# Kernel tuning notes

Hardware: AMD Instinct MI355X
Metric: run time of the kernel (lower is better)

Reference implementation:

```python
import jax, jax.numpy as jnp
import numpy as np

BN_EPS = 1e-5

def _conv(x, w, b, pad):
    # x [B,C,H,W], w [O,I,kh,kw]
    y = jax.lax.conv_general_dilated(x, w, window_strides=(1, 1),
                                     padding=[(pad, pad), (pad, pad)],
                                     dimension_numbers=('NCHW', 'OIHW', 'NCHW'))
    return y + b[None, :, None, None]

def _bn(x, p):
    # p [4,C] rows: gamma, beta, running_mean, running_var (inference-mode BN)
    g, b, m, v = p
    scale = (g * jax.lax.rsqrt(v + BN_EPS))[None, :, None, None]
    return (x - m[None, :, None, None]) * scale + b[None, :, None, None]

def _up2_bilinear_ac(x):
    # UpsamplingBilinear2d(scale_factor=2) == bilinear, align_corners=True
    def interp(x, axis):
        n = x.shape[axis]
        out = 2 * n
        c = jnp.arange(out, dtype=x.dtype) * ((n - 1) / (out - 1))
        i0 = jnp.floor(c).astype(jnp.int32)
        i1 = jnp.minimum(i0 + 1, n - 1)
        w = c - i0.astype(x.dtype)
        sh = [1] * x.ndim
        sh[axis] = out
        w = w.reshape(sh)
        return jnp.take(x, i0, axis=axis) * (1 - w) + jnp.take(x, i1, axis=axis) * w
    return interp(interp(x, 2), 3)

def _dilate(x, k, iterations):
    # cv2.dilate with ones(k,k) kernel == sliding-window max (the custom-kernel target);
    # get_open_map detaches, hence stop_gradient.
    for _ in range(iterations):
        x = jax.lax.reduce_window(x, -jnp.inf, jax.lax.max,
                                  (1, 1, k, k), (1, 1, 1, 1), 'SAME')
    return jax.lax.stop_gradient(x)

def _pixel_shuffle2(x):
    B, C4, H, W = x.shape
    C = C4 // 4
    x = x.reshape(B, C, 2, 2, H, W).transpose(0, 1, 4, 2, 5, 3)
    return x.reshape(B, C, 2 * H, 2 * W)

def setup_inputs() -> dict:
    key = jax.random.key(0)
    ks = jax.random.split(key, 16)
    B, C1, C2, H, W = 8, 64, 128, 64, 64

    def bn_params(k, C):
        k1, k2, k3, k4 = jax.random.split(k, 4)
        g = jax.random.uniform(k1, (C,)) * 0.5 + 0.75
        b = jax.random.normal(k2, (C,)) * 0.1
        m = jax.random.normal(k3, (C,)) * 0.1
        v = jax.random.uniform(k4, (C,)) + 0.5
        return jnp.stack([g, b, m, v])

    def conv_w(k, o, i, kk):
        return jax.random.normal(k, (o, i, kk, kk)) * 0.05

    return {
        'cur_x': jax.random.normal(ks[0], (B, C1, 2 * H, 2 * W)),
        'dep_x': jax.random.normal(ks[1], (B, C2, H, W)),
        'in_map': jax.random.normal(ks[2], (B, 1, H, W)),
        'up_w': conv_w(ks[3], 4 * C1, C2, 7), 'up_b': jnp.zeros((4 * C1,)),
        'up_bn': bn_params(ks[4], 4 * C1),
        'conv2_w': conv_w(ks[5], C1, C1, 3), 'conv2_b': jnp.zeros((C1,)),
        'd1_w': conv_w(ks[6], C1, C1, 3), 'd1_b': jnp.zeros((C1,)),
        'd1_bn': bn_params(ks[7], C1),
        'd2_w': conv_w(ks[8], C1, C1, 3), 'd2_b': jnp.zeros((C1,)),
        'd2_bn': bn_params(ks[9], C1),
        'd3_w': conv_w(ks[10], C1, C1, 3), 'd3_b': jnp.zeros((C1,)),
        'd3_bn': bn_params(ks[11], C1),
        'out_w': conv_w(ks[12], 1, C1, 7), 'out_b': jnp.zeros((1,)),
        'beta': jnp.ones((1,)),
    }

def reference(cur_x, dep_x, in_map, up_w, up_b, up_bn, conv2_w, conv2_b,
              d1_w, d1_b, d1_bn, d2_w, d2_b, d2_bn, d3_w, d3_b, d3_bn,
              out_w, out_b, beta):
    K, IT = 3, 1  # opr_kernel_size, iterations
    # up + pixel shuffle: [B,C2,H,W] -> [B,C1,2H,2W]
    dep = _pixel_shuffle2(jax.nn.relu(_bn(_conv(dep_x, up_w, up_b, 3), up_bn)))
    in_map1 = 1.0 - in_map
    input_map = jax.nn.sigmoid(_up2_bilinear_ac(in_map))
    input_map1 = jax.nn.sigmoid(_up2_bilinear_ac(in_map1))
    increase_map = _dilate(input_map, K, IT) - input_map
    increase_map1 = _dilate(increase_map, K, IT) - increase_map
    increase_map2 = _dilate(input_map1, K, IT) - input_map1
    outmap = increase_map + increase_map1 + increase_map2
    fn = _conv(outmap * cur_x, conv2_w, conv2_b, 1)
    r = jax.nn.relu(_bn(_conv(dep + beta * fn, d1_w, d1_b, 1), d1_bn))
    r = jax.nn.relu(_bn(_conv(r, d2_w, d2_b, 1), d2_bn))
    r = jax.nn.relu(_bn(_conv(r, d3_w, d3_b, 1), d3_bn))
    output_map = _conv(r, out_w, out_b, 3)
    return (r, output_map)
```

## Files before the change

### kernel.cpp

```cpp
#include <hip/hip_runtime.h>
#include <hip/hip_bf16.h>
#include <math.h>

static __device__ __forceinline__ float sigm(float x) { return 1.0f / (1.0f + expf(-x)); }

static __device__ __forceinline__ short f2bf_s(float f) {
    unsigned u = __float_as_uint(f);
    u += 0x7fffu + ((u >> 16) & 1u);
    return (short)(u >> 16);
}
static __device__ __forceinline__ float bfb2f(short s) {
    return __uint_as_float(((unsigned)(unsigned short)s) << 16);
}

typedef __attribute__((ext_vector_type(8))) short short8;
typedef __attribute__((ext_vector_type(4))) short short4v;
typedef __attribute__((ext_vector_type(4))) float f32x4;

__global__ __launch_bounds__(256) void k_maps(const float* __restrict__ in_map,
                                              short* __restrict__ om_bf) {
    __shared__ float s_u[20][20];
    __shared__ float s_inc[18][18];
    int tid = threadIdx.x;
    int b = blockIdx.z;
    int ty0 = (blockIdx.x >> 3) << 4, tx0 = (blockIdx.x & 7) << 4;
    const float* p = in_map + (b << 12);
    const float s = 63.0f / 127.0f;
    for (int e = tid; e < 400; e += 256) {
        int yy = e / 20, xx = e % 20;
        int gy = ty0 + yy - 2, gx = tx0 + xx - 2;
        float v = 0.0f;
        if ((unsigned)gy < 128u && (unsigned)gx < 128u) {
            float cy = gy * s, cx = gx * s;
            int iy0 = (int)cy, ix0 = (int)cx;
            float wy = cy - (float)iy0, wx = cx - (float)ix0;
            int iy1 = min(iy0 + 1, 63), ix1 = min(ix0 + 1, 63);
            float v00 = p[(iy0 << 6) + ix0], v01 = p[(iy0 << 6) + ix1];
            float v10 = p[(iy1 << 6) + ix0], v11 = p[(iy1 << 6) + ix1];
            v = (1.0f - wy) * ((1.0f - wx) * v00 + wx * v01) +
                wy          * ((1.0f - wx) * v10 + wx * v11);
        }
        s_u[yy][xx] = v;
    }
    __syncthreads();
    for (int e = tid; e < 324; e += 256) {
        int yy = e / 18, xx = e % 18;
        int gy = ty0 + yy - 1, gx = tx0 + xx - 1;
        float val = -INFINITY;
        if ((unsigned)gy < 128u && (unsigned)gx < 128u) {
            float uc = s_u[yy + 1][xx + 1];
            float mx = -INFINITY;
            for (int dy = -1; dy <= 1; ++dy) {
                int ny = gy + dy; if ((unsigned)ny >= 128u) continue;
                for (int dx = -1; dx <= 1; ++dx) {
                    int nx = gx + dx; if ((unsigned)nx >= 128u) continue;
                    mx = fmaxf(mx, s_u[yy + 1 + dy][xx + 1 + dx]);
                }
            }
            val = sigm(mx) - sigm(uc);
        }
        s_inc[yy][xx] = val;
    }
    __syncthreads();
    int row = tid >> 4, col = tid & 15;
    int gy = ty0 + row, gx = tx0 + col;
    float mx = -INFINITY;
    #pragma unroll
    for (int dy = 0; dy < 3; ++dy)
        #pragma unroll
        for (int dx = 0; dx < 3; ++dx)
            mx = fmaxf(mx, s_inc[row + dy][col + dx]);
    float uc = s_u[row + 2][col + 2];
    float mn = INFINITY;
    for (int dy = -1; dy <= 1; ++dy) {
        int ny = gy + dy; if ((unsigned)ny >= 128u) continue;
        for (int dx = -1; dx <= 1; ++dx) {
            int nx = gx + dx; if ((unsigned)nx >= 128u) continue;
            mn = fminf(mn, s_u[row + 2 + dy][col + 2 + dx]);
        }
    }
    float inc2 = sigm(1.0f - mn) - sigm(1.0f - uc);
    om_bf[(b << 14) + (gy << 7) + gx] = f2bf_s(mx + inc2);
}

__global__ __launch_bounds__(256) void k_premult(const float* __restrict__ cur_x,
                                                 const short* __restrict__ om_bf,
                                                 short* __restrict__ xin2) {
    int e = blockIdx.x * 256 + threadIdx.x;
    int flat = e << 2;
    int pix = flat & 16383;
    int b = flat >> 20;
    f32x4 xv = *(const f32x4*)&cur_x[flat];
    short4v ov = *(const short4v*)&om_bf[(b << 14) + pix];
    short4v res;
    #pragma unroll
    for (int k = 0; k < 4; ++k) res[k] = f2bf_s(xv[k] * bfb2f(ov[k]));
    *(short4v*)&xin2[flat] = res;
}

__global__ __launch_bounds__(256) void k_prepw3(const float* __restrict__ w0,
                                                const float* __restrict__ w1,
                                                const float* __restrict__ w2,
                                                const float* __restrict__ w3,
                                                short* __restrict__ wb3) {
    int s = blockIdx.x * 256 + threadIdx.x;
    if (s >= 147456) return;
    int layer = s / 36864; int r = s - layer * 36864;
    const float* w = (layer == 0) ? w0 : (layer == 1) ? w1 : (layer == 2) ? w2 : w3;
    int o = r / 576; int rem = r - o * 576;
    int c = rem / 9; int t = rem - c * 9;
    int dy = t / 3, dx = t - dy * 3;
    int cc = c >> 5, cl = c & 31;
    wb3[layer * 36864 + (((cc * 3 + dy) * 3 + dx) * 64 + o) * 32 + cl] = f2bf_s(w[r]);
}

__global__ __launch_bounds__(256) void k_prepw(const float* __restrict__ w,
                                               short* __restrict__ wb) {
    int s = blockIdx.x * 256 + threadIdx.x;
    if (s >= 1605632) return;
    int O = s / 6272; int r = s - O * 6272;
    int C = r / 49;   int T = r - C * 49;
    int dy = T / 7, dx = T - dy * 7;
    int nt = O >> 6, o = O & 63;
    int cc = C >> 5, c = C & 31;
    int W = ((((nt * 4 + cc) * 7 + dy) * 7 + dx) * 64 + o) * 32 + c;
    wb[W] = f2bf_s(w[s]);
}

__global__ __launch_bounds__(512) void k_upconv_mfma(
    const float* __restrict__ x,
    const short* __restrict__ wb,
    const float* __restrict__ cb,
    const float* __restrict__ bnp,
    short* __restrict__ dep) {
    __shared__ __attribute__((aligned(16))) short s_in[484 * 40];
    int tid = threadIdx.x;
    int wave = tid >> 6, lane = tid & 63;
    int q = lane >> 4, m = lane & 15;
    int mw = wave & 3, ng = wave >> 2;
    int ty0 = (blockIdx.x >> 2) * 16;
    int tx0 = (blockIdx.x & 3) * 16;
    int nt = blockIdx.y;
    int b = blockIdx.z;
    f32x4 acc[4][2];
    #pragma unroll
    for (int i = 0; i < 4; ++i)
        #pragma unroll
        for (int j = 0; j < 2; ++j)
            acc[i][j] = (f32x4){0.f, 0.f, 0.f, 0.f};
    const float* xb = x + ((long)(b * 128) << 12);
    for (int cc = 0; cc < 4; ++cc) {
        __syncthreads();
        for (int e = tid; e < 528; e += 512) {
            int cq = e / 132; int rem = e - cq * 132;
            int yy = rem / 6; int g = rem - yy * 6;
            int gy = ty0 + yy - 3;
            int gx0 = tx0 - 4 + (g << 2);
            bool ok = ((unsigned)gy < 64u) && ((unsigned)gx0 < 64u);
            #pragma unroll
            for (int h = 0; h < 2; ++h) {
                f32x4 v[4];
                if (ok) {
                    const float* src = xb + ((cc * 32 + cq * 8 + h * 4) << 12) + (gy << 6) + gx0;
                    #pragma unroll
                    for (int j2 = 0; j2 < 4; ++j2) v[j2] = *(const f32x4*)(src + (j2 << 12));
                } else {
                    #pragma unroll
                    for (int j2 = 0; j2 < 4; ++j2) v[j2] = (f32x4){0.f, 0.f, 0.f, 0.f};
                }
                #pragma unroll
                for (int t = 0; t < 4; ++t) {
                    int xx = (g << 2) - 1 + t;
                    if ((unsigned)xx < 22u) {
                        short4v pk;
                        #pragma unroll
                        for (int j2 = 0; j2 < 4; ++j2) pk[j2] = f2bf_s(v[j2][t]);
                        *(short4v*)&s_in[(yy * 22 + xx) * 40 + cq * 8 + h * 4] = pk;
                    }
                }
            }
        }
        __syncthreads();
        for (int dy = 0; dy < 7; ++dy) {
            const short* wsl = wb + (((nt * 4 + cc) * 7 + dy) * 7) * 2048;
            #pragma unroll
            for (int dx = 0; dx < 7; ++dx) {
                short8 bf[2];
                #pragma unroll
                for (int j = 0; j < 2; ++j)
                    bf[j] = *(const short8*)(wsl + (dx << 11) + ((ng * 32 + j * 16 + m) << 5) + (q << 3));
                short8 a[4];
                #pragma unroll
                for (int i = 0; i < 4; ++i)
                    a[i] = *(const short8*)&s_in[((mw * 4 + i + dy) * 22 + m + dx) * 40 + q * 8];
                #pragma unroll
                for (int i = 0; i < 4; ++i)
                    #pragma unroll
                    for (int j = 0; j < 2; ++j)
                        acc[i][j] = __builtin_amdgcn_mfma_f32_16x16x32_bf16(
                            a[i], bf[j], acc[i][j], 0, 0, 0);
            }
        }
    }
    #pragma unroll
    for (int j = 0; j < 2; ++j) {
        int o = nt * 64 + ng * 32 + j * 16 + m;
        float g  = bnp[o],       bt = bnp[256 + o];
        float mn = bnp[512 + o], vv = bnp[768 + o];
        float scale = g * rsqrtf(vv + 1e-5f);
        float cbf = cb[o];
        int c = o >> 2, sbit = (o >> 1) & 1, tbit = o & 1;
        #pragma unroll
        for (int i = 0; i < 4; ++i) {
            int y = ty0 + mw * 4 + i;
            #pragma unroll
            for (int reg = 0; reg < 4; ++reg) {
                int xc = tx0 + q * 4 + reg;
                float val = (acc[i][j][reg] + cbf - mn) * scale + bt;
                val = fmaxf(val, 0.0f);
                dep[((b * 64 + c) << 14) + ((2 * y + sbit) << 7) + (2 * xc + tbit)] = f2bf_s(val);
            }
        }
    }
}

template <int MODE, bool OUTBF>
__global__ __launch_bounds__(256) void k_conv3m(
    const short* __restrict__ xin,
    const short* __restrict__ wl,
    const short* __restrict__ dep,
    const float* __restrict__ cb,
    const float* __restrict__ bnp,
    const float* __restrict__ beta,
    void* __restrict__ out) {
    __shared__ __attribute__((aligned(16))) short s_in[180 * 40];
    int tid = threadIdx.x;
    int wave = tid >> 6, lane = tid & 63;
    int q = lane >> 4, m = lane & 15;
    int mw = wave >> 1, nw = wave & 1;
    int ty0 = (blockIdx.x >> 3) * 8;
    int tx0 = (blockIdx.x & 7) * 16;
    int b = blockIdx.z;
    f32x4 acc[4][2];
    #pragma unroll
    for (int i = 0; i < 4; ++i)
        #pragma unroll
        for (int j = 0; j < 2; ++j)
            acc[i][j] = (f32x4){0.f, 0.f, 0.f, 0.f};
    const short* xb = xin + ((long)(b * 64) << 14);
    for (int cc = 0; cc < 2; ++cc) {
        __syncthreads();
        for (int e = tid; e < 240; e += 256) {
            int cq = e / 60; int rem = e - cq * 60;
            int yy = rem / 6; int g = rem - yy * 6;
            int gy = ty0 + yy - 1;
            int gx0 = tx0 - 4 + (g << 2);
            short4v v[8];
            if ((unsigned)gy < 128u && (unsigned)gx0 < 128u) {
                const short* src = xb + ((cc * 32 + cq * 8) << 14) + (gy << 7) + gx0;
                #pragma unroll
                for (int j2 = 0; j2 < 8; ++j2) v[j2] = *(const short4v*)(src + (j2 << 14));
            } else {
                #pragma unroll
                for (int j2 = 0; j2 < 8; ++j2) v[j2] = (short4v){0, 0, 0, 0};
            }
            #pragma unroll
            for (int t = 0; t < 4; ++t) {
                int xx = (g << 2) - 3 + t;
                if ((unsigned)xx < 18u) {
                    short8 pk;
                    #pragma unroll
                    for (int j2 = 0; j2 < 8; ++j2) pk[j2] = v[j2][t];
                    *(short8*)&s_in[(yy * 18 + xx) * 40 + cq * 8] = pk;
                }
            }
        }
        __syncthreads();
        #pragma unroll
        for (int dy = 0; dy < 3; ++dy) {
            #pragma unroll
            for (int dx = 0; dx < 3; ++dx) {
                const short* wp = wl + (((cc * 3 + dy) * 3 + dx) << 11);
                short8 bf[2];
                #pragma unroll
                for (int j = 0; j < 2; ++j)
                    bf[j] = *(const short8*)(wp + ((nw * 32 + j * 16 + m) << 5) + (q << 3));
                short8 a[4];
                #pragma unroll
                for (int i = 0; i < 4; ++i)
                    a[i] = *(const short8*)&s_in[((mw * 4 + i + dy) * 18 + m + dx) * 40 + q * 8];
                #pragma unroll
                for (int i = 0; i < 4; ++i)
                    #pragma unroll
                    for (int j = 0; j < 2; ++j)
                        acc[i][j] = __builtin_amdgcn_mfma_f32_16x16x32_bf16(
                            a[i], bf[j], acc[i][j], 0, 0, 0);
            }
        }
    }
    float betav = (MODE == 1) ? beta[0] : 0.0f;
    #pragma unroll
    for (int j = 0; j < 2; ++j) {
        int o = nw * 32 + j * 16 + m;
        float cbf = cb[o];
        float scale = 1.0f, shift = 0.0f;
        if (MODE == 0) {
            float g  = bnp[o],       bt = bnp[64 + o];
            float mm = bnp[128 + o], vv = bnp[192 + o];
            scale = g * rsqrtf(vv + 1e-5f);
            shift = bt - mm * scale;
        }
        #pragma unroll
        for (int i = 0; i < 4; ++i) {
            int y = ty0 + mw * 4 + i;
            int base = ((b * 64 + o) << 14) + (y << 7) + tx0 + q * 4;
            float vals[4];
            if (MODE == 1) {
                short4v dv = *(const short4v*)&dep[base];
                #pragma unroll
                for (int reg = 0; reg < 4; ++reg)
                    vals[reg] = bfb2f(dv[reg]) + betav * (acc[i][j][reg] + cbf);
            } else {
                #pragma unroll
                for (int reg = 0; reg < 4; ++reg)
                    vals[reg] = fmaxf((acc[i][j][reg] + cbf) * scale + shift, 0.0f);
            }
            if (OUTBF) {
                short4v sv;
                #pragma unroll
                for (int reg = 0; reg < 4; ++reg) sv[reg] = f2bf_s(vals[reg]);
                *(short4v*)((short*)out + base) = sv;
            } else {
                f32x4 fv;
                #pragma unroll
                for (int reg = 0; reg < 4; ++reg) fv[reg] = vals[reg];
                *(f32x4*)((float*)out + base) = fv;
            }
        }
    }
}

__global__ __launch_bounds__(256) void k_outconv(
    const float* __restrict__ r,
    const float* __restrict__ w,
    const float* __restrict__ ob,
    float* __restrict__ out) {
    __shared__ float s_in[8][22][22];
    int tid = threadIdx.x;
    int ty = tid >> 4, tx = tid & 15;
    int ty0 = (blockIdx.x >> 3) << 4, tx0 = (blockIdx.x & 7) << 4;
    int b = blockIdx.z;
    float acc4[4] = {0.f, 0.f, 0.f, 0.f};
    for (int c0 = 0; c0 < 64; c0 += 8) {
        __syncthreads();
        for (int e = tid; e < 8 * 484; e += 256) {
            int i = e / 484; int r2 = e - i * 484; int yy = r2 / 22; int xx = r2 - yy * 22;
            int gy = ty0 + yy - 3, gx = tx0 + xx - 3;
            float v = 0.0f;
            if ((unsigned)gy < 128u && (unsigned)gx < 128u)
                v = r[((b * 64 + c0 + i) << 14) + (gy << 7) + gx];
            s_in[i][yy][xx] = v;
        }
        __syncthreads();
        for (int i = 0; i < 8; ++i) {
            const float* wrow = w + (c0 + i) * 49;
            #pragma unroll
            for (int dy = 0; dy < 7; ++dy)
                #pragma unroll
                for (int dx = 0; dx < 7; ++dx)
                    acc4[i & 3] = fmaf(s_in[i][ty + dy][tx + dx], wrow[dy * 7 + dx], acc4[i & 3]);
        }
    }
    out[(b << 14) + ((ty0 + ty) << 7) + tx0 + tx] =
        (acc4[0] + acc4[1]) + (acc4[2] + acc4[3]) + ob[0];
}

extern "C" void kernel_launch(void* const* d_in, const int* in_sizes, int n_in,
                              void* d_out, int out_size, void* d_ws, size_t ws_size,
                              hipStream_t stream) {
    const float* cur_x  = (const float*)d_in[0];
    const float* dep_x  = (const float*)d_in[1];
    const float* in_map = (const float*)d_in[2];
    const float* up_w   = (const float*)d_in[3];
    const float* up_b   = (const float*)d_in[4];
    const float* up_bn  = (const float*)d_in[5];
    const float* c2_w   = (const float*)d_in[6];
    const float* c2_b   = (const float*)d_in[7];
    const float* d1_w   = (const float*)d_in[8];
    const float* d1_b   = (const float*)d_in[9];
    const float* d1_bn  = (const float*)d_in[10];
    const float* d2_w   = (const float*)d_in[11];
    const float* d2_b   = (const float*)d_in[12];
    const float* d2_bn  = (const float*)d_in[13];
    const float* d3_w   = (const float*)d_in[14];
    const float* d3_b   = (const float*)d_in[15];
    const float* d3_bn  = (const float*)d_in[16];
    const float* out_w  = (const float*)d_in[17];
    const float* out_b  = (const float*)d_in[18];
    const float* beta   = (const float*)d_in[19];

    char* ob = (char*)d_out;
    float* r_out  = (float*)ob;
    short* A      = (short*)d_ws;
    short* B      = (short*)ob;
    short* C      = (short*)(ob + 16777216);
    short* wb     = C;
    short* om_bf  = (short*)(ob + 33554432);
    short* wb3    = (short*)(ob + 33554432);
    float* mapout = (float*)(ob + 33554432);

    k_maps<<<dim3(64, 1, 8), 256, 0, stream>>>(in_map, om_bf);
    k_premult<<<8192, 256, 0, stream>>>(cur_x, om_bf, A);
    k_prepw3<<<576, 256, 0, stream>>>(c2_w, d1_w, d2_w, d3_w, wb3);
    k_prepw<<<6272, 256, 0, stream>>>(up_w, wb);
    k_upconv_mfma<<<dim3(16, 4, 8), 512, 0, stream>>>(dep_x, wb, up_b, up_bn, B);
    k_conv3m<1, true><<<dim3(128, 1, 8), 256, 0, stream>>>(
        A, wb3 + 0 * 36864, B, c2_b, nullptr, beta, C);
    k_conv3m<0, true><<<dim3(128, 1, 8), 256, 0, stream>>>(
        C, wb3 + 1 * 36864, nullptr, d1_b, d1_bn, nullptr, B);
    k_conv3m<0, true><<<dim3(128, 1, 8), 256, 0, stream>>>(
        B, wb3 + 2 * 36864, nullptr, d2_b, d2_bn, nullptr, A);
    k_conv3m<0, false><<<dim3(128, 1, 8), 256, 0, stream>>>(
        A, wb3 + 3 * 36864, nullptr, d3_b, d3_bn, nullptr, r_out);
    k_outconv<<<dim3(64, 1, 8), 256, 0, stream>>>(r_out, out_w, out_b, mapout);
}
```

Measured before the change: 467.5 us.

## Pre-pack padded bf16 input and double-buffer upconv tiles via global_load_lds

Adds a prepass kernel that converts dep_x to a zero-padded, channel-blocked bf16 layout, so the 7x7 upconv can stage input tiles with direct global-to-LDS 16-byte loads. The LDS tile is double-buffered so the next channel chunk loads while MFMAs run on the current one, removing the per-block fp32 load and convert work. This costs an extra kernel launch, roughly 12.5MB of extra global writes and reads, and doubled LDS use, which may reduce occupancy. Correctness depends on the async LDS loads being waited on before the barrier.

```diff
diff --git a/kernel.cpp b/kernel.cpp
--- a/kernel.cpp
+++ b/kernel.cpp
@@ -16,6 +16,12 @@
 typedef __attribute__((ext_vector_type(8))) short short8;
 typedef __attribute__((ext_vector_type(4))) short short4v;
 typedef __attribute__((ext_vector_type(4))) float f32x4;
+
+static __device__ __forceinline__ void gl_lds16(const void* g, void* l) {
+    __builtin_amdgcn_global_load_lds(
+        (const __attribute__((address_space(1))) unsigned int*)g,
+        (__attribute__((address_space(3))) unsigned int*)l, 16, 0, 0);
+}
 
 __global__ __launch_bounds__(256) void k_maps(const float* __restrict__ in_map,
                                               short* __restrict__ om_bf) {
@@ -127,13 +133,36 @@
     wb[W] = f2bf_s(w[s]);
 }
 
+__global__ __launch_bounds__(256) void k_prepx(const float* __restrict__ x,
+                                               short* __restrict__ px) {
+    int b = blockIdx.z;
+    int yp = blockIdx.x;
+    int tid = threadIdx.x;
+    int y = yp - 3;
+    bool inY = (unsigned)y < 64u;
+    for (int cc = 0; cc < 4; ++cc) {
+        short* orow = px + (((long)(b * 4 + cc) * 70 + yp) * 70) * 40;
+        for (int e = tid; e < 350; e += 256) {
+            int p = e / 70, xp = e - p * 70;
+            int xg = xp - 3;
+            short8 v = (short8){0, 0, 0, 0, 0, 0, 0, 0};
+            if (p < 4 && inY && (unsigned)xg < 64u) {
+                const float* src = x + (((b * 128 + cc * 32 + p * 8) << 12)) + (y << 6) + xg;
+                #pragma unroll
+                for (int i = 0; i < 8; ++i) v[i] = f2bf_s(src[i << 12]);
+            }
+            *(short8*)&orow[xp * 40 + p * 8] = v;
+        }
+    }
+}
+
 __global__ __launch_bounds__(512) void k_upconv_mfma(
-    const float* __restrict__ x,
+    const short* __restrict__ px,
     const short* __restrict__ wb,
     const float* __restrict__ cb,
     const float* __restrict__ bnp,
     short* __restrict__ dep) {
-    __shared__ __attribute__((aligned(16))) short s_in[484 * 40];
+    __shared__ __attribute__((aligned(16))) short s_in[2][19360];
     int tid = threadIdx.x;
     int wave = tid >> 6, lane = tid & 63;
     int q = lane >> 4, m = lane & 15;
@@ -148,39 +177,23 @@
         #pragma unroll
         for (int j = 0; j < 2; ++j)
             acc[i][j] = (f32x4){0.f, 0.f, 0.f, 0.f};
-    const float* xb = x + ((long)(b * 128) << 12);
+
+    auto stage = [&](int cc, int bsel) {
+        const short* pxcc = px + ((((long)(b * 4 + cc) * 70 + ty0) * 70 + tx0) * 40);
+        for (int c0 = (wave << 6); c0 < 2420; c0 += 512) {
+            int chunk = c0 + lane;
+            int row = chunk / 110;
+            int k = chunk - row * 110;
+            if (chunk < 2420)
+                gl_lds16(pxcc + row * 2800 + (k << 3), &s_in[bsel][c0 << 3]);
+        }
+    };
+
+    stage(0, 0);
     for (int cc = 0; cc < 4; ++cc) {
         __syncthreads();
-        for (int e = tid; e < 528; e += 512) {
-            int cq = e / 132; int rem = e - cq * 132;
-            int yy = rem / 6; int g = rem - yy * 6;
-            int gy = ty0 + yy - 3;
-            int gx0 = tx0 - 4 + (g << 2);
-            bool ok = ((unsigned)gy < 64u) && ((unsigned)gx0 < 64u);
-            #pragma unroll
-            for (int h = 0; h < 2; ++h) {
-                f32x4 v[4];
-                if (ok) {
-                    const float* src = xb + ((cc * 32 + cq * 8 + h * 4) << 12) + (gy << 6) + gx0;
-                    #pragma unroll
-                    for (int j2 = 0; j2 < 4; ++j2) v[j2] = *(const f32x4*)(src + (j2 << 12));
-                } else {
-                    #pragma unroll
-                    for (int j2 = 0; j2 < 4; ++j2) v[j2] = (f32x4){0.f, 0.f, 0.f, 0.f};
-                }
-                #pragma unroll
-                for (int t = 0; t < 4; ++t) {
-                    int xx = (g << 2) - 1 + t;
-                    if ((unsigned)xx < 22u) {
-                        short4v pk;
-                        #pragma unroll
-                        for (int j2 = 0; j2 < 4; ++j2) pk[j2] = f2bf_s(v[j2][t]);
-                        *(short4v*)&s_in[(yy * 22 + xx) * 40 + cq * 8 + h * 4] = pk;
-                    }
-                }
-            }
-        }
-        __syncthreads();
+        if (cc < 3) stage(cc + 1, (cc + 1) & 1);
+        const short* sb = &s_in[cc & 1][0];
         for (int dy = 0; dy < 7; ++dy) {
             const short* wsl = wb + (((nt * 4 + cc) * 7 + dy) * 7) * 2048;
             #pragma unroll
@@ -192,7 +205,7 @@
                 short8 a[4];
                 #pragma unroll
                 for (int i = 0; i < 4; ++i)
-                    a[i] = *(const short8*)&s_in[((mw * 4 + i + dy) * 22 + m + dx) * 40 + q * 8];
+                    a[i] = *(const short8*)&sb[((mw * 4 + i + dy) * 22 + m + dx) * 40 + q * 8];
                 #pragma unroll
                 for (int i = 0; i < 4; ++i)
                     #pragma unroll
@@ -405,6 +418,7 @@
     short* B      = (short*)ob;
     short* C      = (short*)(ob + 16777216);
     short* wb     = C;
+    short* px     = wb + 1605632;
     short* om_bf  = (short*)(ob + 33554432);
     short* wb3    = (short*)(ob + 33554432);
     float* mapout = (float*)(ob + 33554432);
@@ -413,7 +427,8 @@
     k_premult<<<8192, 256, 0, stream>>>(cur_x, om_bf, A);
     k_prepw3<<<576, 256, 0, stream>>>(c2_w, d1_w, d2_w, d3_w, wb3);
     k_prepw<<<6272, 256, 0, stream>>>(up_w, wb);
-    k_upconv_mfma<<<dim3(16, 4, 8), 512, 0, stream>>>(dep_x, wb, up_b, up_bn, B);
+    k_prepx<<<dim3(70, 1, 8), 256, 0, stream>>>(dep_x, px);
+    k_upconv_mfma<<<dim3(16, 4, 8), 512, 0, stream>>>(px, wb, up_b, up_bn, B);
     k_conv3m<1, true><<<dim3(128, 1, 8), 256, 0, stream>>>(
         A, wb3 + 0 * 36864, B, c2_b, nullptr, beta, C);
     k_conv3m<0, true><<<dim3(128, 1, 8), 256, 0, stream>>>(
```

Result: no change. 470.5 us (+0.6%).
